# Kernel optimization log

Measured on AMD Instinct MI355X. Metric: run time of the kernel, lower is better.

The kernel has to match this reference:

```python
import jax, jax.numpy as jnp
import numpy as np

L = 24        # n_layer
E = 1024      # n_emb
H = 4 * E     # ffn hidden
V = 50277     # vocab
LN_EPS = 1e-5


def _ln(x, w, b):
    m = x.mean(-1, keepdims=True)
    v = ((x - m) ** 2).mean(-1, keepdims=True)
    return (x - m) / jnp.sqrt(v + LN_EPS) * w + b


def setup_inputs() -> dict:
    key = jax.random.key(0)
    ks = jax.random.split(key, 24)
    s = 1.0 / np.sqrt(E)      # keep matvec outputs O(1) so exp-recurrence is stable
    sh = 1.0 / np.sqrt(H)
    inp = {
        "emb":      jax.random.normal(ks[0], (V, E), jnp.float32) * 0.02,
        "ln0_w":    jnp.ones((E,), jnp.float32),
        "ln0_b":    jnp.zeros((E,), jnp.float32),
        "ln1_w":    jnp.ones((L, E), jnp.float32),
        "ln1_b":    jnp.zeros((L, E), jnp.float32),
        "att_tmk":  jax.random.uniform(ks[1], (L, E), jnp.float32),
        "att_tmv":  jax.random.uniform(ks[2], (L, E), jnp.float32),
        "att_tmr":  jax.random.uniform(ks[3], (L, E), jnp.float32),
        "att_tf":   jax.random.normal(ks[4], (L, E), jnp.float32) * 0.3,
        # checkpoint stores raw time_decay; loader applies -exp(.)
        "att_td":   -jnp.exp(jax.random.normal(ks[5], (L, E), jnp.float32) * 0.3),
        "att_kw":   jax.random.normal(ks[6], (L, E, E), jnp.float32) * s,
        "att_vw":   jax.random.normal(ks[7], (L, E, E), jnp.float32) * s,
        "att_rw":   jax.random.normal(ks[8], (L, E, E), jnp.float32) * s,
        "att_ow":   jax.random.normal(ks[9], (L, E, E), jnp.float32) * s,
        "ln2_w":    jnp.ones((L, E), jnp.float32),
        "ln2_b":    jnp.zeros((L, E), jnp.float32),
        "ffn_tmk":  jax.random.uniform(ks[10], (L, E), jnp.float32),
        "ffn_tmr":  jax.random.uniform(ks[11], (L, E), jnp.float32),
        "ffn_kw":   jax.random.normal(ks[12], (L, H, E), jnp.float32) * s,
        "ffn_vw":   jax.random.normal(ks[13], (L, E, H), jnp.float32) * sh,
        "ffn_rw":   jax.random.normal(ks[14], (L, E, E), jnp.float32) * s,
        "ln_out_w": jnp.ones((E,), jnp.float32),
        "ln_out_b": jnp.zeros((E,), jnp.float32),
        "head_w":   jax.random.normal(ks[15], (V, E), jnp.float32) * s,
        "token":    123,
    }
    state = jnp.zeros((5 * L, E), jnp.float32)
    state = state.at[4::5].set(-1e30)  # pp slot, as in empty_state()
    inp["state"] = state
    return inp


def _rwkv_forward(emb, ln0_w, ln0_b, ln1_w, ln1_b, att_tmk, att_tmv, att_tmr,
                  att_tf, att_td, att_kw, att_vw, att_rw, att_ow,
                  ln2_w, ln2_b, ffn_tmk, ffn_tmr, ffn_kw, ffn_vw, ffn_rw,
                  ln_out_w, ln_out_b, head_w, state, token):
    x = emb[token]
    x = _ln(x, ln0_w, ln0_b)           # blocks.0.ln0 applied once before layer 0
    st = state.reshape(L, 5, E)        # slots: (ffn_x, att_x, aa, bb, pp)

    def step(x, inp):
        (s, l1w, l1b, tmk, tmv, tmr, tf, td, kw, vw, rw, ow,
         l2w, l2b, ftmk, ftmr, fkw, fvw, frw) = inp
        ffn_x, att_x, aa, bb, pp = s[0], s[1], s[2], s[3], s[4]
        # --- time-mix (SA) ---
        xn = _ln(x, l1w, l1b)
        xk = xn * tmk + att_x * (1 - tmk)
        xv = xn * tmv + att_x * (1 - tmv)
        xr = xn * tmr + att_x * (1 - tmr)
        r = jax.nn.sigmoid(rw @ xr)
        k = kw @ xk
        v = vw @ xv
        # numerically-stabilized WKV output
        ww = tf + k
        p = jnp.maximum(pp, ww)
        e1 = jnp.exp(pp - p)
        e2 = jnp.exp(ww - p)
        a = e1 * aa + e2 * v
        b = e1 * bb + e2
        # state update
        ww2 = pp + td
        p2 = jnp.maximum(ww2, k)
        f1 = jnp.exp(ww2 - p2)
        f2 = jnp.exp(k - p2)
        naa = f1 * aa + f2 * v
        nbb = f1 * bb + f2
        npp = p2
        sx = x + ow @ (r * a / b)
        # --- channel-mix (FF) ---
        xn2 = _ln(sx, l2w, l2b)
        fxk = xn2 * ftmk + ffn_x * (1 - ftmk)
        fxr = xn2 * ftmr + ffn_x * (1 - ftmr)
        fr = jax.nn.sigmoid(frw @ fxr)
        fk = jnp.square(jax.nn.relu(fkw @ fxk))
        out = sx + fr * (fvw @ fk)
        new_s = jnp.stack([xn2, xn, naa, nbb, npp])
        return out, new_s

    xs = (st, ln1_w, ln1_b, att_tmk, att_tmv, att_tmr, att_tf, att_td,
          att_kw, att_vw, att_rw, att_ow, ln2_w, ln2_b, ffn_tmk, ffn_tmr,
          ffn_kw, ffn_vw, ffn_rw)
    x, new_st = jax.lax.scan(step, x, xs)
    logits = head_w @ _ln(x, ln_out_w, ln_out_b)
    return logits, new_st.reshape(5 * L, E)


def reference(emb, ln0_w, ln0_b, ln1_w, ln1_b, att_tmk, att_tmv, att_tmr,
              att_tf, att_td, att_kw, att_vw, att_rw, att_ow,
              ln2_w, ln2_b, ffn_tmk, ffn_tmr, ffn_kw, ffn_vw, ffn_rw,
              ln_out_w, ln_out_b, head_w, state, token):
    return _rwkv_forward(emb, ln0_w, ln0_b, ln1_w, ln1_b, att_tmk, att_tmv,
                         att_tmr, att_tf, att_td, att_kw, att_vw, att_rw,
                         att_ow, ln2_w, ln2_b, ffn_tmk, ffn_tmr, ffn_kw,
                         ffn_vw, ffn_rw, ln_out_w, ln_out_b, head_w,
                         state, token)
```

## Files before the change

kernel.cpp:

```cpp
#include <hip/hip_runtime.h>

#define E 1024
#define H 4096
#define NLAYER 24
#define V 50277
#define NB 256
#define NT 1024
#define LN_EPS 1e-5f

typedef unsigned long long u64;

#define R1O    0
#define R2O    16384
#define POOLO  32768
#define SXO    36864
#define SSXO   37888
#define FXRO   38912
#define REDO   39936
#define PARTO  39968
#define PART2O 39984
#define SMEMF  40000

struct Params {
  const float* emb;   const float* ln0_w; const float* ln0_b;
  const float* ln1_w; const float* ln1_b;
  const float* tmk;   const float* tmv;   const float* tmr;
  const float* tf;    const float* td;
  const float* kw;    const float* vw;    const float* rw;  const float* ow;
  const float* ln2_w; const float* ln2_b;
  const float* ftmk;  const float* ftmr;
  const float* fkw;   const float* fvw;   const float* frw;
  const float* lnow;  const float* lnob;  const float* headw;
  const float* st;    const int* tok;
  float* out; float* ws;
};

__device__ __forceinline__ void stg_tag(u64* p, float v, unsigned tag) {
  u64 w = ((u64)__float_as_uint(v) << 32) | (u64)tag;
  __hip_atomic_store(p, w, __ATOMIC_RELAXED, __HIP_MEMORY_SCOPE_AGENT);
}
__device__ __forceinline__ u64 ld_tag(const u64* p) {
  return __hip_atomic_load(p, __ATOMIC_RELAXED, __HIP_MEMORY_SCOPE_AGENT);
}
__device__ __forceinline__ float poll_tag(const u64* p, unsigned tag) {
  u64 w = ld_tag(p);
  while ((unsigned)w != tag) { __builtin_amdgcn_s_sleep(1); w = ld_tag(p); }
  return __uint_as_float((unsigned)(w >> 32));
}

__device__ __forceinline__ void wait_pf() {
  asm volatile("s_waitcnt vmcnt(0)" ::: "memory");
}

__device__ __forceinline__ void gload_lds16(const float* g, float* l) {
  __builtin_amdgcn_global_load_lds(
      (const __attribute__((address_space(1))) unsigned int*)(g),
      (__attribute__((address_space(3))) unsigned int*)(l), 16, 0, 0);
}
__device__ __forceinline__ void pf_row4k(const float* row, float* dst, int lane) {
#pragma unroll
  for (int c = 0; c < 4; ++c)
    gload_lds16(row + c * 256 + lane * 4, dst + c * 256);
}

__device__ __forceinline__ float warp_sum(float v) {
#pragma unroll
  for (int off = 32; off; off >>= 1) v += __shfl_down(v, off);
  return v;
}

__device__ __forceinline__ float2 ln_stats(float v, float* red) {
  float a = v, b = v * v;
#pragma unroll
  for (int off = 32; off; off >>= 1) { a += __shfl_xor(a, off); b += __shfl_xor(b, off); }
  const int wid = threadIdx.x >> 6, lane = threadIdx.x & 63;
  if (lane == 0) { red[2 * wid] = a; red[2 * wid + 1] = b; }
  __syncthreads();
  float s1 = 0.f, s2 = 0.f;
  const float2* r2 = (const float2*)red;
#pragma unroll
  for (int j = 0; j < 16; ++j) { float2 t = r2[j]; s1 += t.x; s2 += t.y; }
  float m = s1 * (1.f / E);
  return make_float2(m, s2 * (1.f / E) - m * m);
}

__device__ __forceinline__ float dot4(float4 a, float4 b) {
  return a.x * b.x + a.y * b.y + a.z * b.z + a.w * b.w;
}

__device__ __forceinline__ float dotlds(const float* wrow, const float* vec, int lane) {
  const float4* w4 = (const float4*)wrow;
  const float4* v4 = (const float4*)vec;
  float acc = 0.f;
#pragma unroll
  for (int p = 0; p < 4; ++p)
    acc += dot4(w4[lane + p * 64], v4[lane + p * 64]);
  return warp_sum(acc);
}

__global__ __launch_bounds__(NT, 1) void rwkv_kernel(Params p) {
  const int tid = threadIdx.x, bid = blockIdx.x;
  const int lane = tid & 63, wid = tid >> 6;

  extern __shared__ float smem[];
  float* r1     = smem + R1O;
  float* r2     = smem + R2O;
  float* pool   = smem + POOLO;
  float* s_x    = smem + SXO;
  float* s_sx   = smem + SSXO;
  float* s_fxr  = smem + FXRO;
  float* s_red  = smem + REDO;
  float* s_part = smem + PARTO;
  float* s_part2= smem + PART2O;

  u64* tws = (u64*)p.ws;
  u64* twk = tws;
  u64* tsx = tws + 6 * E;
  u64* tx  = tws + 8 * E;
  u64* tfk = tws + 10 * E;

  float* out_st = p.out + V;
  const int token = p.tok[0];

  const bool hasA = wid < 12;
  const int matA = wid >> 2;
  const int rowA = bid * 4 + (wid & 3);
  const int rloc = wid >> 2, kc = wid & 3;
  const int rowO = bid * 4 + rloc;
  float* wA = r1 + wid * 1024;
  float* wD = r2 + rloc * 4096 + kc * 1024;

  if (hasA) {
    const float* W = (matA == 0 ? p.kw : matA == 1 ? p.vw : p.rw) + (size_t)rowA * E;
    pf_row4k(W, wA, lane);
  }

  {
    float v = p.emb[(size_t)token * E + tid];
    float2 mv = ln_stats(v, s_red);
    s_x[tid] = (v - mv.x) / sqrtf(mv.y + LN_EPS) * p.ln0_w[tid] + p.ln0_b[tid];
  }

  for (int l = 0; l < NLAYER; ++l) {
    const float* stl = p.st + (size_t)5 * l * E;
    float* ostl = out_st + (size_t)5 * l * E;
    const int par = l & 1;
    const unsigned tg = (unsigned)(l + 1);

    float l1w = p.ln1_w[l * E + tid], l1b = p.ln1_b[l * E + tid];
    float ax = stl[E + tid];
    float ta = p.tmk[l * E + tid], tb = p.tmv[l * E + tid], tc = p.tmr[l * E + tid];
    float aav, bbv, ppv, tfv, tdv;
    const int eOwn = bid * 4 + tid;
    if (tid < 4) {
      aav = stl[2 * E + eOwn]; bbv = stl[3 * E + eOwn]; ppv = stl[4 * E + eOwn];
      tfv = p.tf[l * E + eOwn]; tdv = p.td[l * E + eOwn];
    }
    float xv_;
    if (l > 0) { xv_ = poll_tag(&tx[par * E + tid], (unsigned)l); s_x[tid] = xv_; }
    else       { xv_ = s_x[tid]; }
    {
      float2 mv = ln_stats(xv_, s_red);
      float xn = (xv_ - mv.x) / sqrtf(mv.y + LN_EPS) * l1w + l1b;
      pool[tid]        = xn * ta + ax * (1.f - ta);
      pool[1024 + tid] = xn * tb + ax * (1.f - tb);
      pool[2048 + tid] = xn * tc + ax * (1.f - tc);
      if (bid == 0) ostl[E + tid] = xn;
    }
    __syncthreads();
    wait_pf();
    if (hasA) {
      float d = dotlds(wA, pool + matA * 1024, lane);
      if (lane == 0) s_part[wid] = d;
    }
    __syncthreads();
    if (tid < 4) {
      float kk = s_part[tid], vv = s_part[4 + tid];
      float rr = 1.f / (1.f + expf(-s_part[8 + tid]));
      float wwv = tfv + kk;
      float pm = fmaxf(ppv, wwv);
      float e1 = expf(ppv - pm), e2 = expf(wwv - pm);
      float a = e1 * aav + e2 * vv, b = e1 * bbv + e2;
      stg_tag(&twk[par * E + eOwn], rr * a / b, tg);
      float ww2 = ppv + tdv;
      float p2 = fmaxf(ww2, kk);
      float f1 = expf(ww2 - p2), f2 = expf(kk - p2);
      ostl[2 * E + eOwn] = f1 * aav + f2 * vv;
      ostl[3 * E + eOwn] = f1 * bbv + f2;
      ostl[4 * E + eOwn] = p2;
    }

    {
      float4 wow = ((const float4*)(p.ow + (size_t)l * E * E + (size_t)rowO * E + kc * 256))[lane];
      pf_row4k(p.fkw + (size_t)l * H * E + (size_t)(bid * 16 + wid) * E, wA, lane);
      pool[3072 + tid] = poll_tag(&twk[par * E + tid], tg);
      __syncthreads();
      const float4* v4 = (const float4*)(pool + 3072 + kc * 256);
      float acc = warp_sum(dot4(wow, v4[lane]));
      if (lane == 0) s_part[wid] = acc;
    }
    __syncthreads();
    if (tid < 4) {
      float dsum = s_part[tid * 4] + s_part[tid * 4 + 1] +
                   s_part[tid * 4 + 2] + s_part[tid * 4 + 3];
      stg_tag(&tsx[par * E + bid * 4 + tid], s_x[bid * 4 + tid] + dsum, tg);
    }

    {
      float l2w = p.ln2_w[l * E + tid], l2b = p.ln2_b[l * E + tid];
      float fx = stl[tid];
      float fa = p.ftmk[l * E + tid], fb = p.ftmr[l * E + tid];
      float4 wfr = ((const float4*)(p.frw + (size_t)l * E * E + (size_t)rowO * E + kc * 256))[lane];
      pf_row4k(p.fvw + (size_t)l * E * H + (size_t)rowO * H + kc * 1024, wD, lane);
      float sxv = poll_tag(&tsx[par * E + tid], tg);
      s_sx[tid] = sxv;
      float2 mv = ln_stats(sxv, s_red);
      float xn2 = (sxv - mv.x) / sqrtf(mv.y + LN_EPS) * l2w + l2b;
      pool[tid]  = xn2 * fa + fx * (1.f - fa);
      s_fxr[tid] = xn2 * fb + fx * (1.f - fb);
      if (bid == 0) ostl[tid] = xn2;
      __syncthreads();
      float d = dotlds(wA, pool, lane);
      if (lane == 0) { float t = fmaxf(d, 0.f); stg_tag(&tfk[par * H + bid * 16 + wid], t * t, tg); }
      const float4* f4 = (const float4*)(s_fxr + kc * 256);
      float fp = warp_sum(dot4(wfr, f4[lane]));
      if (lane == 0) s_part2[wid] = fp;
    }

    if (l + 1 < NLAYER && hasA) {
      const float* W = (matA == 0 ? p.kw : matA == 1 ? p.vw : p.rw) +
                       (size_t)(l + 1) * E * E + (size_t)rowA * E;
      pf_row4k(W, wA, lane);
    }
    __syncthreads();
    {
      const u64* base = tfk + par * H;
      u64 w0 = ld_tag(base + tid);
      u64 w1 = ld_tag(base + tid + 1024);
      u64 w2 = ld_tag(base + tid + 2048);
      u64 w3 = ld_tag(base + tid + 3072);
      while ((unsigned)w0 != tg) { __builtin_amdgcn_s_sleep(1); w0 = ld_tag(base + tid); }
      while ((unsigned)w1 != tg) { __builtin_amdgcn_s_sleep(1); w1 = ld_tag(base + tid + 1024); }
      while ((unsigned)w2 != tg) { __builtin_amdgcn_s_sleep(1); w2 = ld_tag(base + tid + 2048); }
      while ((unsigned)w3 != tg) { __builtin_amdgcn_s_sleep(1); w3 = ld_tag(base + tid + 3072); }
      pool[tid]        = __uint_as_float((unsigned)(w0 >> 32));
      pool[tid + 1024] = __uint_as_float((unsigned)(w1 >> 32));
      pool[tid + 2048] = __uint_as_float((unsigned)(w2 >> 32));
      pool[tid + 3072] = __uint_as_float((unsigned)(w3 >> 32));
    }
    __syncthreads();
    {
      const float4* v4 = (const float4*)(pool + kc * 1024);
      const float4* w4 = (const float4*)wD;
      float acc = 0.f;
#pragma unroll
      for (int pc = 0; pc < 4; ++pc)
        acc += dot4(w4[lane + pc * 64], v4[lane + pc * 64]);
      acc = warp_sum(acc);
      if (lane == 0) s_part[wid] = acc;
    }
    __syncthreads();
    if (tid < 4) {
      float dsum = s_part[tid * 4] + s_part[tid * 4 + 1] +
                   s_part[tid * 4 + 2] + s_part[tid * 4 + 3];
      float frs  = s_part2[tid * 4] + s_part2[tid * 4 + 1] +
                   s_part2[tid * 4 + 2] + s_part2[tid * 4 + 3];
      float fr = 1.f / (1.f + expf(-frs));
      stg_tag(&tx[((l + 1) & 1) * E + bid * 4 + tid],
              s_sx[bid * 4 + tid] + fr * dsum, tg);
    }
  }

  {
    float xv_ = poll_tag(&tx[(NLAYER & 1) * E + tid], (unsigned)NLAYER);
    float2 mv = ln_stats(xv_, s_red);
    pool[tid] = (xv_ - mv.x) / sqrtf(mv.y + LN_EPS) * p.lnow[tid] + p.lnob[tid];
  }
  __syncthreads();
  {
    const int gw = bid * 16 + wid;
    const float4* v4 = (const float4*)pool;
    float4 x0 = v4[lane], x1 = v4[lane + 64], x2 = v4[lane + 128], x3 = v4[lane + 192];
    int row = gw;
    for (; row + 12288 < V; row += 16384) {
      const float4* W0 = (const float4*)(p.headw + (size_t)row * E);
      const float4* W1 = (const float4*)(p.headw + (size_t)(row + 4096) * E);
      const float4* W2 = (const float4*)(p.headw + (size_t)(row + 8192) * E);
      const float4* W3 = (const float4*)(p.headw + (size_t)(row + 12288) * E);
      float a0 = 0.f, a1 = 0.f, a2 = 0.f, a3 = 0.f;
      a0 += dot4(W0[lane], x0) + dot4(W0[lane + 64], x1) + dot4(W0[lane + 128], x2) + dot4(W0[lane + 192], x3);
      a1 += dot4(W1[lane], x0) + dot4(W1[lane + 64], x1) + dot4(W1[lane + 128], x2) + dot4(W1[lane + 192], x3);
      a2 += dot4(W2[lane], x0) + dot4(W2[lane + 64], x1) + dot4(W2[lane + 128], x2) + dot4(W2[lane + 192], x3);
      a3 += dot4(W3[lane], x0) + dot4(W3[lane + 64], x1) + dot4(W3[lane + 128], x2) + dot4(W3[lane + 192], x3);
      a0 = warp_sum(a0); a1 = warp_sum(a1); a2 = warp_sum(a2); a3 = warp_sum(a3);
      if (lane == 0) {
        p.out[row] = a0; p.out[row + 4096] = a1;
        p.out[row + 8192] = a2; p.out[row + 12288] = a3;
      }
    }
    for (; row < V; row += 4096) {
      const float4* W0 = (const float4*)(p.headw + (size_t)row * E);
      float a0 = dot4(W0[lane], x0) + dot4(W0[lane + 64], x1) +
                 dot4(W0[lane + 128], x2) + dot4(W0[lane + 192], x3);
      a0 = warp_sum(a0);
      if (lane == 0) p.out[row] = a0;
    }
  }
}

extern "C" void kernel_launch(void* const* d_in, const int* in_sizes, int n_in,
                              void* d_out, int out_size, void* d_ws, size_t ws_size,
                              hipStream_t stream) {
  Params p;
  p.emb   = (const float*)d_in[0];
  p.ln0_w = (const float*)d_in[1];
  p.ln0_b = (const float*)d_in[2];
  p.ln1_w = (const float*)d_in[3];
  p.ln1_b = (const float*)d_in[4];
  p.tmk   = (const float*)d_in[5];
  p.tmv   = (const float*)d_in[6];
  p.tmr   = (const float*)d_in[7];
  p.tf    = (const float*)d_in[8];
  p.td    = (const float*)d_in[9];
  p.kw    = (const float*)d_in[10];
  p.vw    = (const float*)d_in[11];
  p.rw    = (const float*)d_in[12];
  p.ow    = (const float*)d_in[13];
  p.ln2_w = (const float*)d_in[14];
  p.ln2_b = (const float*)d_in[15];
  p.ftmk  = (const float*)d_in[16];
  p.ftmr  = (const float*)d_in[17];
  p.fkw   = (const float*)d_in[18];
  p.fvw   = (const float*)d_in[19];
  p.frw   = (const float*)d_in[20];
  p.lnow  = (const float*)d_in[21];
  p.lnob  = (const float*)d_in[22];
  p.headw = (const float*)d_in[23];
  if (in_sizes[24] == 1) {
    p.tok = (const int*)d_in[24];
    p.st  = (const float*)d_in[25];
  } else {
    p.st  = (const float*)d_in[24];
    p.tok = (const int*)d_in[25];
  }
  p.out   = (float*)d_out;
  p.ws    = (float*)d_ws;

  hipMemsetAsync(d_ws, 0, (10 * E + 2 * H) * sizeof(unsigned long long), stream);

  void* args[] = { &p };
  hipLaunchCooperativeKernel((const void*)rwkv_kernel, dim3(NB), dim3(NT),
                             args, SMEMF * sizeof(float), stream);
}
```

Measured before the change: 487.9 us.

## Replace block barriers with LDS atomic counters for per-row reductions

Removes three __syncthreads barriers per layer. The final warp to arrive now finishes each row's reduction through LDS atomicAdd accumulators and arrival counters, and the r-warp spins until the k and v partials are ready before running the WKV update. The aim is to shorten the serial critical path between cross-block tagged stores in a latency-bound persistent kernel. In exchange it adds LDS atomics and intra-block spin-waits, and float atomic accumulation makes the summation order nondeterministic.

```diff
diff --git a/kernel.cpp b/kernel.cpp
--- a/kernel.cpp
+++ b/kernel.cpp
@@ -18,8 +18,11 @@
 #define FXRO   38912
 #define REDO   39936
 #define PARTO  39968
-#define PART2O 39984
-#define SMEMF  40000
+#define BACCO  39984
+#define DACCO  39988
+#define FACCO  39992
+#define CNTO   39996
+#define SMEMF  40008
 
 struct Params {
   const float* emb;   const float* ln0_w; const float* ln0_b;
@@ -111,7 +114,12 @@
   float* s_fxr  = smem + FXRO;
   float* s_red  = smem + REDO;
   float* s_part = smem + PARTO;
-  float* s_part2= smem + PART2O;
+  float* s_bacc = smem + BACCO;
+  float* s_dacc = smem + DACCO;
+  float* s_facc = smem + FACCO;
+  unsigned* s_acnt = (unsigned*)(smem + CNTO);
+  unsigned* s_bcnt = (unsigned*)(smem + CNTO) + 4;
+  unsigned* s_dcnt = (unsigned*)(smem + CNTO) + 8;
 
   u64* tws = (u64*)p.ws;
   u64* twk = tws;
@@ -130,6 +138,8 @@
   float* wA = r1 + wid * 1024;
   float* wD = r2 + rloc * 4096 + kc * 1024;
 
+  if (tid < 24) smem[BACCO + tid] = 0.f;
+
   if (hasA) {
     const float* W = (matA == 0 ? p.kw : matA == 1 ? p.vw : p.rw) + (size_t)rowA * E;
     pf_row4k(W, wA, lane);
@@ -150,9 +160,9 @@
     float l1w = p.ln1_w[l * E + tid], l1b = p.ln1_b[l * E + tid];
     float ax = stl[E + tid];
     float ta = p.tmk[l * E + tid], tb = p.tmv[l * E + tid], tc = p.tmr[l * E + tid];
-    float aav, bbv, ppv, tfv, tdv;
-    const int eOwn = bid * 4 + tid;
-    if (tid < 4) {
+    float aav = 0.f, bbv = 0.f, ppv = 0.f, tfv = 0.f, tdv = 0.f;
+    const int eOwn = bid * 4 + (wid & 3);
+    if (wid >= 8 && wid < 12 && lane == 0) {
       aav = stl[2 * E + eOwn]; bbv = stl[3 * E + eOwn]; ppv = stl[4 * E + eOwn];
       tfv = p.tf[l * E + eOwn]; tdv = p.td[l * E + eOwn];
     }
@@ -171,23 +181,30 @@
     wait_pf();
     if (hasA) {
       float d = dotlds(wA, pool + matA * 1024, lane);
-      if (lane == 0) s_part[wid] = d;
-    }
-    __syncthreads();
-    if (tid < 4) {
-      float kk = s_part[tid], vv = s_part[4 + tid];
-      float rr = 1.f / (1.f + expf(-s_part[8 + tid]));
-      float wwv = tfv + kk;
-      float pm = fmaxf(ppv, wwv);
-      float e1 = expf(ppv - pm), e2 = expf(wwv - pm);
-      float a = e1 * aav + e2 * vv, b = e1 * bbv + e2;
-      stg_tag(&twk[par * E + eOwn], rr * a / b, tg);
-      float ww2 = ppv + tdv;
-      float p2 = fmaxf(ww2, kk);
-      float f1 = expf(ww2 - p2), f2 = expf(kk - p2);
-      ostl[2 * E + eOwn] = f1 * aav + f2 * vv;
-      ostl[3 * E + eOwn] = f1 * bbv + f2;
-      ostl[4 * E + eOwn] = p2;
+      if (matA < 2) {
+        if (lane == 0) {
+          s_part[wid] = d;
+          atomicAdd(&s_acnt[wid & 3], 1u);
+        }
+      } else if (lane == 0) {
+        const int e = wid & 3;
+        while (*(volatile unsigned*)&s_acnt[e] < 2u) __builtin_amdgcn_s_sleep(1);
+        asm volatile("" ::: "memory");
+        float kk = s_part[e], vv = s_part[4 + e];
+        float rr = 1.f / (1.f + expf(-d));
+        float wwv = tfv + kk;
+        float pm = fmaxf(ppv, wwv);
+        float e1 = expf(ppv - pm), e2 = expf(wwv - pm);
+        float a = e1 * aav + e2 * vv, b = e1 * bbv + e2;
+        stg_tag(&twk[par * E + eOwn], rr * a / b, tg);
+        float ww2 = ppv + tdv;
+        float p2 = fmaxf(ww2, kk);
+        float f1 = expf(ww2 - p2), f2 = expf(kk - p2);
+        ostl[2 * E + eOwn] = f1 * aav + f2 * vv;
+        ostl[3 * E + eOwn] = f1 * bbv + f2;
+        ostl[4 * E + eOwn] = p2;
+        *(volatile unsigned*)&s_acnt[e] = 0u;
+      }
     }
 
     {
@@ -197,13 +214,17 @@
       __syncthreads();
       const float4* v4 = (const float4*)(pool + 3072 + kc * 256);
       float acc = warp_sum(dot4(wow, v4[lane]));
-      if (lane == 0) s_part[wid] = acc;
-    }
-    __syncthreads();
-    if (tid < 4) {
-      float dsum = s_part[tid * 4] + s_part[tid * 4 + 1] +
-                   s_part[tid * 4 + 2] + s_part[tid * 4 + 3];
-      stg_tag(&tsx[par * E + bid * 4 + tid], s_x[bid * 4 + tid] + dsum, tg);
+      if (lane == 0) {
+        atomicAdd(&s_bacc[rloc], acc);
+        unsigned old = atomicAdd(&s_bcnt[rloc], 1u);
+        if (old == 3u) {
+          asm volatile("" ::: "memory");
+          float dsum = *(volatile float*)&s_bacc[rloc];
+          stg_tag(&tsx[par * E + bid * 4 + rloc], s_x[bid * 4 + rloc] + dsum, tg);
+          *(volatile float*)&s_bacc[rloc] = 0.f;
+          *(volatile unsigned*)&s_bcnt[rloc] = 0u;
+        }
+      }
     }
 
     {
@@ -224,7 +245,7 @@
       if (lane == 0) { float t = fmaxf(d, 0.f); stg_tag(&tfk[par * H + bid * 16 + wid], t * t, tg); }
       const float4* f4 = (const float4*)(s_fxr + kc * 256);
       float fp = warp_sum(dot4(wfr, f4[lane]));
-      if (lane == 0) s_part2[wid] = fp;
+      if (lane == 0) atomicAdd(&s_facc[rloc], fp);
     }
 
     if (l + 1 < NLAYER && hasA) {
@@ -257,17 +278,21 @@
       for (int pc = 0; pc < 4; ++pc)
         acc += dot4(w4[lane + pc * 64], v4[lane + pc * 64]);
       acc = warp_sum(acc);
-      if (lane == 0) s_part[wid] = acc;
-    }
-    __syncthreads();
-    if (tid < 4) {
-      float dsum = s_part[tid * 4] + s_part[tid * 4 + 1] +
-                   s_part[tid * 4 + 2] + s_part[tid * 4 + 3];
-      float frs  = s_part2[tid * 4] + s_part2[tid * 4 + 1] +
-                   s_part2[tid * 4 + 2] + s_part2[tid * 4 + 3];
-      float fr = 1.f / (1.f + expf(-frs));
-      stg_tag(&tx[((l + 1) & 1) * E + bid * 4 + tid],
-              s_sx[bid * 4 + tid] + fr * dsum, tg);
+      if (lane == 0) {
+        atomicAdd(&s_dacc[rloc], acc);
+        unsigned old = atomicAdd(&s_dcnt[rloc], 1u);
+        if (old == 3u) {
+          asm volatile("" ::: "memory");
+          float dsum = *(volatile float*)&s_dacc[rloc];
+          float frs  = *(volatile float*)&s_facc[rloc];
+          float fr = 1.f / (1.f + expf(-frs));
+          stg_tag(&tx[((l + 1) & 1) * E + bid * 4 + rloc],
+                  s_sx[bid * 4 + rloc] + fr * dsum, tg);
+          *(volatile float*)&s_dacc[rloc] = 0.f;
+          *(volatile float*)&s_facc[rloc] = 0.f;
+          *(volatile unsigned*)&s_dcnt[rloc] = 0u;
+        }
+      }
     }
   }
 
```

After: 674.0 us. 38.1% more time.
